# Optimization experiments

Hardware: AMD Instinct MI355X
Metric: run time of the kernel (lower is better)

The kernel has to match this reference:

```python
import jax, jax.numpy as jnp
import numpy as np

BATCH = 256
SIZE = 512      # must be a power of two for the bitonic network
K = 16          # top-k
STEEPNESS = 10.0  # cauchy distribution scale (module default)


def _bitonic_layers(n):
    """Static index pairs of the bitonic sorting network (ascending).
    Returns (lefts, rights), each int32 [n_layers, n//2]. After a compare-swap,
    the soft-min goes to `left` and the soft-max goes to `right`."""
    lefts, rights = [], []
    k = 2
    while k <= n:
        j = k // 2
        while j >= 1:
            l_idx, r_idx = [], []
            for i in range(n):
                l = i ^ j
                if l > i:
                    if (i & k) == 0:   # ascending block: min at i
                        l_idx.append(i); r_idx.append(l)
                    else:              # descending block: min at l
                        l_idx.append(l); r_idx.append(i)
            lefts.append(l_idx); rights.append(r_idx)
            j //= 2
        k *= 2
    return np.asarray(lefts, np.int32), np.asarray(rights, np.int32)


def setup_inputs() -> dict:
    key = jax.random.key(0)
    vectors = jax.random.normal(key, (BATCH, SIZE), dtype=jnp.float32)
    return {"vectors": vectors}


def reference(vectors):
    b, n = vectors.shape
    lefts_np, rights_np = _bitonic_layers(n)
    lefts = jnp.asarray(lefts_np)
    rights = jnp.asarray(rights_np)
    # soft permutation matrix: X[b, i, j] = P(input j ends at sorted pos i)
    X0 = jnp.broadcast_to(jnp.eye(n, dtype=vectors.dtype)[None], (b, n, n))

    def step(carry, lr):
        x, X = carry
        l, r = lr                      # [n//2] index pairs for this layer
        a = x[:, l]                    # [b, n//2]
        c = x[:, r]
        # cauchy CDF of steepness*(c - a): prob that no swap is needed
        alpha = jnp.arctan((c - a) * STEEPNESS) / jnp.pi + 0.5
        x = x.at[:, l].set(alpha * a + (1.0 - alpha) * c)
        x = x.at[:, r].set(alpha * c + (1.0 - alpha) * a)
        Xl = X[:, l, :]                # [b, n//2, n]
        Xr = X[:, r, :]
        al = alpha[..., None]
        X = X.at[:, l, :].set(al * Xl + (1.0 - al) * Xr)
        X = X.at[:, r, :].set(al * Xr + (1.0 - al) * Xl)
        return (x, X), None

    (_, X), _ = jax.lax.scan(step, (vectors, X0), (lefts, rights))
    # ascending sort -> last K rows correspond to the K largest elements;
    # flip so row 0 = largest. Output: [batch, K, n] soft top-k distribution.
    return jnp.flip(X[:, n - K:, :], axis=1)
```

## Files before the change

### kernel.cpp

```cpp
#include <hip/hip_runtime.h>
#include <math.h>

#define N 512
#define BATCH 256
#define KTOP 16
#define NLAYERS 45
#define NPAIRS 256

__global__ __launch_bounds__(256, 1)
void difftopk_kernel(const float* __restrict__ x_in, float* __restrict__ out) {
    __shared__ float xs[N];
    __shared__ float As[NLAYERS * NPAIRS];

    const int b   = blockIdx.x;
    const int tid = threadIdx.x;

    xs[tid]       = x_in[(size_t)b * N + tid];
    xs[tid + 256] = x_in[(size_t)b * N + tid + 256];
    __syncthreads();

    int t = 0;
    for (int k = 2; k <= N; k <<= 1) {
        for (int j = k >> 1; j >= 1; j >>= 1) {
            const int low = tid & (j - 1);
            const int i   = ((tid ^ low) << 1) | low;
            const int p   = i | j;
            int left, right;
            if ((i & k) == 0) { left = i; right = p; }
            else              { left = p; right = i; }
            const float a = xs[left];
            const float c = xs[right];
            const float alpha = atanf((c - a) * 10.0f) * 0.3183098861837907f + 0.5f;
            As[t * NPAIRS + tid] = alpha;
            xs[left]  = alpha * a + (1.0f - alpha) * c;
            xs[right] = alpha * c + (1.0f - alpha) * a;
            ++t;
            __syncthreads();
        }
    }

    const int wave  = tid >> 6;
    const int lane  = tid & 63;
    const int lane8 = lane << 3;

    float v[4][8];
    #pragma unroll
    for (int c = 0; c < 4; ++c) {
        const int r = N - 1 - (wave * 4 + c);
        #pragma unroll
        for (int m = 0; m < 8; ++m) v[c][m] = (lane8 + m == r) ? 1.0f : 0.0f;
    }

    #pragma unroll
    for (int kk_ = 9; kk_ >= 1; --kk_) {
        #pragma unroll
        for (int lg = 0; lg < kk_; ++lg) {
            const int j  = 1 << lg;
            const int tt = ((kk_ - 1) * kk_) / 2 + (kk_ - 1 - lg);
            float al[8];
            #pragma unroll
            for (int m = 0; m < 8; ++m) {
                const int i   = lane8 + m;
                const int ord = ((i >> (lg + 1)) << lg) | (i & (j - 1));
                al[m] = As[tt * NPAIRS + ord];
            }
            if (j >= 8) {
                const int lm = j >> 3;
                #pragma unroll
                for (int c = 0; c < 4; ++c) {
                    #pragma unroll
                    for (int m = 0; m < 8; ++m) {
                        const float part = __shfl_xor(v[c][m], lm, 64);
                        v[c][m] = al[m] * v[c][m] + (1.0f - al[m]) * part;
                    }
                }
            } else {
                #pragma unroll
                for (int c = 0; c < 4; ++c) {
                    float nv[8];
                    #pragma unroll
                    for (int m = 0; m < 8; ++m)
                        nv[m] = al[m] * v[c][m] + (1.0f - al[m]) * v[c][m ^ j];
                    #pragma unroll
                    for (int m = 0; m < 8; ++m) v[c][m] = nv[m];
                }
            }
        }
    }

    #pragma unroll
    for (int c = 0; c < 4; ++c) {
        const int kk = wave * 4 + c;
        float4* dst = (float4*)(out + ((size_t)b * KTOP + kk) * N + lane8);
        dst[0] = make_float4(v[c][0], v[c][1], v[c][2], v[c][3]);
        dst[1] = make_float4(v[c][4], v[c][5], v[c][6], v[c][7]);
    }
}

extern "C" void kernel_launch(void* const* d_in, const int* in_sizes, int n_in,
                              void* d_out, int out_size, void* d_ws, size_t ws_size,
                              hipStream_t stream) {
    const float* x = (const float*)d_in[0];
    float* out = (float*)d_out;
    difftopk_kernel<<<dim3(BATCH), dim3(256), 0, stream>>>(x, out);
}
```

Before: 79.31 us.

## Use 1024-thread blocks with per-element forward pass and one output row per wave

Expands each block from 256 to 1024 threads. In the forward network, 512 threads each own one element in a register and use a ping-pong shared buffer. In the backward pass, 16 waves each compute one of the K output rows instead of 4 waves handling 4 rows each. Alpha values are loaded as float4 vectors, and the layer loops are no longer unrolled, which shrinks code and register use. The cost is that half the threads sit idle during the serial forward pass, and synchronisation now spans a larger block.

```diff
diff --git a/kernel.cpp b/kernel.cpp
--- a/kernel.cpp
+++ b/kernel.cpp
@@ -7,34 +7,43 @@
 #define NLAYERS 45
 #define NPAIRS 256
 
-__global__ __launch_bounds__(256, 1)
+__global__ __launch_bounds__(1024, 1)
 void difftopk_kernel(const float* __restrict__ x_in, float* __restrict__ out) {
-    __shared__ float xs[N];
-    __shared__ float As[NLAYERS * NPAIRS];
+    __shared__ float xs[2][N];
+    __shared__ __align__(16) float As[NLAYERS][NPAIRS];
 
     const int b   = blockIdx.x;
     const int tid = threadIdx.x;
 
-    xs[tid]       = x_in[(size_t)b * N + tid];
-    xs[tid + 256] = x_in[(size_t)b * N + tid + 256];
+    float o = 0.0f;
+    if (tid < N) {
+        o = x_in[(size_t)b * N + tid];
+        xs[0][tid] = o;
+    }
     __syncthreads();
 
+    int cur = 0;
     int t = 0;
-    for (int k = 2; k <= N; k <<= 1) {
-        for (int j = k >> 1; j >= 1; j >>= 1) {
-            const int low = tid & (j - 1);
-            const int i   = ((tid ^ low) << 1) | low;
-            const int p   = i | j;
-            int left, right;
-            if ((i & k) == 0) { left = i; right = p; }
-            else              { left = p; right = i; }
-            const float a = xs[left];
-            const float c = xs[right];
-            const float alpha = atanf((c - a) * 10.0f) * 0.3183098861837907f + 0.5f;
-            As[t * NPAIRS + tid] = alpha;
-            xs[left]  = alpha * a + (1.0f - alpha) * c;
-            xs[right] = alpha * c + (1.0f - alpha) * a;
-            ++t;
+    #pragma unroll 1
+    for (int s = 1; s <= 9; ++s) {
+        const int k = 1 << s;
+        #pragma unroll 1
+        for (int lg = s - 1; lg >= 0; --lg, ++t) {
+            if (tid < N) {
+                const int e = tid;
+                const int j = 1 << lg;
+                const float p = xs[cur][e ^ j];
+                const bool left = ((e & k) == 0) == ((e & j) == 0);
+                const float d = left ? (p - o) : (o - p);
+                const float alpha = atanf(d * 10.0f) * 0.3183098861837907f + 0.5f;
+                o = alpha * o + (1.0f - alpha) * p;
+                xs[cur ^ 1][e] = o;
+                if ((e & j) == 0) {
+                    const int ord = ((e >> (lg + 1)) << lg) | (e & (j - 1));
+                    As[t][ord] = alpha;
+                }
+            }
+            cur ^= 1;
             __syncthreads();
         }
     }
@@ -42,59 +51,63 @@
     const int wave  = tid >> 6;
     const int lane  = tid & 63;
     const int lane8 = lane << 3;
+    const int r     = N - 1 - wave;
 
-    float v[4][8];
+    float v[8];
     #pragma unroll
-    for (int c = 0; c < 4; ++c) {
-        const int r = N - 1 - (wave * 4 + c);
-        #pragma unroll
-        for (int m = 0; m < 8; ++m) v[c][m] = (lane8 + m == r) ? 1.0f : 0.0f;
-    }
+    for (int m = 0; m < 8; ++m) v[m] = (lane8 + m == r) ? 1.0f : 0.0f;
 
-    #pragma unroll
-    for (int kk_ = 9; kk_ >= 1; --kk_) {
-        #pragma unroll
-        for (int lg = 0; lg < kk_; ++lg) {
-            const int j  = 1 << lg;
-            const int tt = ((kk_ - 1) * kk_) / 2 + (kk_ - 1 - lg);
-            float al[8];
-            #pragma unroll
-            for (int m = 0; m < 8; ++m) {
-                const int i   = lane8 + m;
-                const int ord = ((i >> (lg + 1)) << lg) | (i & (j - 1));
-                al[m] = As[tt * NPAIRS + ord];
-            }
-            if (j >= 8) {
+    #pragma unroll 1
+    for (int s = 9; s >= 1; --s) {
+        const int base = (s * (s - 1)) >> 1;
+        #pragma unroll 1
+        for (int lg = 0; lg < s; ++lg) {
+            const int tt = base + (s - 1 - lg);
+            if (lg >= 3) {
+                const int j    = 1 << lg;
+                const int ordb = ((lane8 >> (lg + 1)) << lg) | (lane8 & (j - 1));
+                const float4 a0 = *(const float4*)&As[tt][ordb];
+                const float4 a1 = *(const float4*)&As[tt][ordb + 4];
+                float al[8] = {a0.x, a0.y, a0.z, a0.w, a1.x, a1.y, a1.z, a1.w};
                 const int lm = j >> 3;
+                float part[8];
                 #pragma unroll
-                for (int c = 0; c < 4; ++c) {
+                for (int m = 0; m < 8; ++m) part[m] = __shfl_xor(v[m], lm, 64);
+                #pragma unroll
+                for (int m = 0; m < 8; ++m)
+                    v[m] = al[m] * v[m] + (1.0f - al[m]) * part[m];
+            } else {
+                const float4 a = *(const float4*)&As[tt][lane << 2];
+                const float aa[4] = {a.x, a.y, a.z, a.w};
+                float nv[8];
+                if (lg == 2) {
                     #pragma unroll
                     for (int m = 0; m < 8; ++m) {
-                        const float part = __shfl_xor(v[c][m], lm, 64);
-                        v[c][m] = al[m] * v[c][m] + (1.0f - al[m]) * part;
+                        const float al = aa[m & 3];
+                        nv[m] = al * v[m] + (1.0f - al) * v[m ^ 4];
+                    }
+                } else if (lg == 1) {
+                    #pragma unroll
+                    for (int m = 0; m < 8; ++m) {
+                        const float al = aa[((m >> 2) << 1) | (m & 1)];
+                        nv[m] = al * v[m] + (1.0f - al) * v[m ^ 2];
+                    }
+                } else {
+                    #pragma unroll
+                    for (int m = 0; m < 8; ++m) {
+                        const float al = aa[m >> 1];
+                        nv[m] = al * v[m] + (1.0f - al) * v[m ^ 1];
                     }
                 }
-            } else {
                 #pragma unroll
-                for (int c = 0; c < 4; ++c) {
-                    float nv[8];
-                    #pragma unroll
-                    for (int m = 0; m < 8; ++m)
-                        nv[m] = al[m] * v[c][m] + (1.0f - al[m]) * v[c][m ^ j];
-                    #pragma unroll
-                    for (int m = 0; m < 8; ++m) v[c][m] = nv[m];
-                }
+                for (int m = 0; m < 8; ++m) v[m] = nv[m];
             }
         }
     }
 
-    #pragma unroll
-    for (int c = 0; c < 4; ++c) {
-        const int kk = wave * 4 + c;
-        float4* dst = (float4*)(out + ((size_t)b * KTOP + kk) * N + lane8);
-        dst[0] = make_float4(v[c][0], v[c][1], v[c][2], v[c][3]);
-        dst[1] = make_float4(v[c][4], v[c][5], v[c][6], v[c][7]);
-    }
+    float4* dst = (float4*)(out + ((size_t)b * KTOP + wave) * N + lane8);
+    dst[0] = make_float4(v[0], v[1], v[2], v[3]);
+    dst[1] = make_float4(v[4], v[5], v[6], v[7]);
 }
 
 extern "C" void kernel_launch(void* const* d_in, const int* in_sizes, int n_in,
@@ -102,5 +115,5 @@
                               hipStream_t stream) {
     const float* x = (const float*)d_in[0];
     float* out = (float*)d_out;
-    difftopk_kernel<<<dim3(BATCH), dim3(256), 0, stream>>>(x, out);
+    difftopk_kernel<<<dim3(BATCH), dim3(1024), 0, stream>>>(x, out);
 }
```

New measurement: 86.60 us. 9.2% more time.
